# Optimization experiments

Hardware: AMD Instinct MI355X
Metric: run time of the kernel (lower is better)

The kernel has to match this reference:

```python
import jax, jax.numpy as jnp
import numpy as np

DIM = 1024
N_HEADS = 16
HEAD_DIM = DIM // N_HEADS
D_FF = 4096
EPS = 1e-6


def setup_inputs() -> dict:
    key = jax.random.key(0)
    ks = jax.random.split(key, 8)
    B, S = 2, 2048
    s = 0.02
    return {
        "x": jax.random.normal(ks[0], (B, S, DIM), dtype=jnp.float32),
        "mask": jnp.ones((B, 1, S, S), dtype=bool),
        "wq": jax.random.normal(ks[1], (DIM, DIM), dtype=jnp.float32) * s,
        "wk": jax.random.normal(ks[2], (DIM, DIM), dtype=jnp.float32) * s,
        "wv": jax.random.normal(ks[3], (DIM, DIM), dtype=jnp.float32) * s,
        "wo": jax.random.normal(ks[4], (DIM, DIM), dtype=jnp.float32) * s,
        "w_up": jax.random.normal(ks[5], (DIM, D_FF), dtype=jnp.float32) * s,
        "b_up": jnp.zeros((D_FF,), dtype=jnp.float32),
        "w_down": jax.random.normal(ks[6], (D_FF, DIM), dtype=jnp.float32) * s,
        "b_down": jnp.zeros((DIM,), dtype=jnp.float32),
        "ln1_a": jnp.ones((DIM,), dtype=jnp.float32),
        "ln1_b": jnp.zeros((DIM,), dtype=jnp.float32),
        "ln2_a": jnp.ones((DIM,), dtype=jnp.float32),
        "ln2_b": jnp.zeros((DIM,), dtype=jnp.float32),
    }


def _layernorm(x, alpha, bias):
    mu = jnp.mean(x, axis=-1, keepdims=True)
    # torch .std() is unbiased (ddof=1); denominator is (std + eps)
    sig = jnp.std(x, axis=-1, keepdims=True, ddof=1)
    return alpha * (x - mu) / (sig + EPS) + bias


def _attention(h, wq, wk, wv, wo):
    B, S, _ = h.shape
    q = (h @ wq).reshape(B, S, N_HEADS, HEAD_DIM).transpose(0, 2, 1, 3)
    k = (h @ wk).reshape(B, S, N_HEADS, HEAD_DIM).transpose(0, 2, 1, 3)
    v = (h @ wv).reshape(B, S, N_HEADS, HEAD_DIM).transpose(0, 2, 1, 3)
    scores = jnp.einsum("bhqd,bhkd->bhqk", q, k) / jnp.sqrt(jnp.float32(HEAD_DIM))
    # NOTE: original's masked_fill result is discarded -> mask is a no-op
    probs = jax.nn.softmax(scores, axis=-1)
    out = jnp.einsum("bhqk,bhkd->bhqd", probs, v)
    out = out.transpose(0, 2, 1, 3).reshape(B, S, DIM)
    return out @ wo


def reference(x, mask, wq, wk, wv, wo, w_up, b_up, w_down, b_down,
              ln1_a, ln1_b, ln2_a, ln2_b):
    h = _layernorm(x, ln1_a, ln1_b)
    x = x + _attention(h, wq, wk, wv, wo)
    h = _layernorm(x, ln2_a, ln2_b)
    ff = (jax.nn.relu(h @ w_up + b_up)) @ w_down + b_down
    return x + ff
```

## Files before the change

### kernel.cpp

```cpp
#include <hip/hip_runtime.h>
#include <hip/hip_bf16.h>

typedef __bf16 bf16_t;
typedef __bf16 bf16x8 __attribute__((ext_vector_type(8)));
typedef __bf16 bf16x4 __attribute__((ext_vector_type(4)));
typedef float  f32x4  __attribute__((ext_vector_type(4)));

#define DIM   1024
#define NHEAD 16
#define HD    64
#define DFF   4096
#define SEQ   2048
#define NTOK  4096

__device__ __forceinline__ void gl_lds16(const bf16_t* g, bf16_t* l) {
  __builtin_amdgcn_global_load_lds(
      (const __attribute__((address_space(1))) void*)g,
      (__attribute__((address_space(3))) void*)l, 16, 0, 0);
}

struct P4 { const float* a; const float* b; const float* c; const float* d; };

__global__ __launch_bounds__(256)
void transpose_cvt4(P4 in, bf16_t* __restrict__ out) {
  __shared__ bf16_t tile[32][33];
  const int z = blockIdx.z;
  const float* src = (z == 0) ? in.a : (z == 1) ? in.b : (z == 2) ? in.c : in.d;
  bf16_t* dst = out + (long)z * DIM * DIM;
  const int bx = blockIdx.x * 32, by = blockIdx.y * 32;
  const int t = threadIdx.x;
  const int r = t >> 3, c4 = (t & 7) * 4;
  f32x4 v = *(const f32x4*)&src[(long)(by + r) * DIM + bx + c4];
  tile[r][c4 + 0] = (bf16_t)v[0]; tile[r][c4 + 1] = (bf16_t)v[1];
  tile[r][c4 + 2] = (bf16_t)v[2]; tile[r][c4 + 3] = (bf16_t)v[3];
  __syncthreads();
  bf16x4 w;
  w[0] = tile[c4 + 0][r]; w[1] = tile[c4 + 1][r];
  w[2] = tile[c4 + 2][r]; w[3] = tile[c4 + 3][r];
  *(bf16x4*)&dst[(long)(bx + r) * DIM + by + c4] = w;
}

__global__ __launch_bounds__(256)
void transpose_cvt(const float* __restrict__ in, bf16_t* __restrict__ out,
                   int M, int N) {
  __shared__ bf16_t tile[32][33];
  const int bx = blockIdx.x * 32, by = blockIdx.y * 32;
  const int t = threadIdx.x;
  const int r = t >> 3, c4 = (t & 7) * 4;
  f32x4 v = *(const f32x4*)&in[(long)(by + r) * N + bx + c4];
  tile[r][c4 + 0] = (bf16_t)v[0]; tile[r][c4 + 1] = (bf16_t)v[1];
  tile[r][c4 + 2] = (bf16_t)v[2]; tile[r][c4 + 3] = (bf16_t)v[3];
  __syncthreads();
  bf16x4 w;
  w[0] = tile[c4 + 0][r]; w[1] = tile[c4 + 1][r];
  w[2] = tile[c4 + 2][r]; w[3] = tile[c4 + 3][r];
  *(bf16x4*)&out[(long)(bx + r) * M + by + c4] = w;
}

__global__ __launch_bounds__(256)
void layernorm_k(const float* __restrict__ x, const float* __restrict__ a,
                 const float* __restrict__ b, bf16_t* __restrict__ out) {
  const int row = blockIdx.x;
  const int t   = threadIdx.x;
  const float* xr = x + (long)row * DIM;
  f32x4 v = *(const f32x4*)&xr[t * 4];
  float s1 = v[0] + v[1] + v[2] + v[3];
  float s2 = v[0]*v[0] + v[1]*v[1] + v[2]*v[2] + v[3]*v[3];
  #pragma unroll
  for (int off = 32; off > 0; off >>= 1) {
    s1 += __shfl_down(s1, off);
    s2 += __shfl_down(s2, off);
  }
  __shared__ float r1[4], r2[4];
  if ((t & 63) == 0) { r1[t >> 6] = s1; r2[t >> 6] = s2; }
  __syncthreads();
  s1 = r1[0] + r1[1] + r1[2] + r1[3];
  s2 = r2[0] + r2[1] + r2[2] + r2[3];
  const float mu = s1 * (1.0f / DIM);
  float var = (s2 - (float)DIM * mu * mu) * (1.0f / (DIM - 1));
  var = fmaxf(var, 0.0f);
  const float inv = 1.0f / (sqrtf(var) + 1e-6f);
  f32x4 av = *(const f32x4*)&a[t * 4];
  f32x4 bv = *(const f32x4*)&b[t * 4];
  bf16x4 o;
  o[0] = (bf16_t)(av[0] * (v[0] - mu) * inv + bv[0]);
  o[1] = (bf16_t)(av[1] * (v[1] - mu) * inv + bv[1]);
  o[2] = (bf16_t)(av[2] * (v[2] - mu) * inv + bv[2]);
  o[3] = (bf16_t)(av[3] * (v[3] - mu) * inv + bv[3]);
  *(bf16x4*)&out[(long)row * DIM + t * 4] = o;
}

__global__ __launch_bounds__(256)
void layernorm_b(const bf16_t* __restrict__ x, const float* __restrict__ a,
                 const float* __restrict__ b, bf16_t* __restrict__ out) {
  const int row = blockIdx.x;
  const int t   = threadIdx.x;
  bf16x4 xv = *(const bf16x4*)&x[(long)row * DIM + t * 4];
  float v0 = (float)xv[0], v1 = (float)xv[1], v2 = (float)xv[2], v3 = (float)xv[3];
  float s1 = v0 + v1 + v2 + v3;
  float s2 = v0*v0 + v1*v1 + v2*v2 + v3*v3;
  #pragma unroll
  for (int off = 32; off > 0; off >>= 1) {
    s1 += __shfl_down(s1, off);
    s2 += __shfl_down(s2, off);
  }
  __shared__ float r1[4], r2[4];
  if ((t & 63) == 0) { r1[t >> 6] = s1; r2[t >> 6] = s2; }
  __syncthreads();
  s1 = r1[0] + r1[1] + r1[2] + r1[3];
  s2 = r2[0] + r2[1] + r2[2] + r2[3];
  const float mu = s1 * (1.0f / DIM);
  float var = (s2 - (float)DIM * mu * mu) * (1.0f / (DIM - 1));
  var = fmaxf(var, 0.0f);
  const float inv = 1.0f / (sqrtf(var) + 1e-6f);
  f32x4 av = *(const f32x4*)&a[t * 4];
  f32x4 bv = *(const f32x4*)&b[t * 4];
  bf16x4 o;
  o[0] = (bf16_t)(av[0] * (v0 - mu) * inv + bv[0]);
  o[1] = (bf16_t)(av[1] * (v1 - mu) * inv + bv[1]);
  o[2] = (bf16_t)(av[2] * (v2 - mu) * inv + bv[2]);
  o[3] = (bf16_t)(av[3] * (v3 - mu) * inv + bv[3]);
  *(bf16x4*)&out[(long)row * DIM + t * 4] = o;
}

__global__ __launch_bounds__(256)
void combine_att(const bf16_t* __restrict__ O1, const float* __restrict__ l0,
                 const float* __restrict__ l1, bf16_t* __restrict__ O0_attn) {
  const long i = ((long)blockIdx.x * 256 + threadIdx.x) * 4;
  const int n = (int)(i & (DIM - 1));
  const long t = i >> 10;
  const int h = n >> 6;
  const long lidx = ((t >> 11) * NHEAD + h) * SEQ + (t & (SEQ - 1));
  const float inv = 1.0f / (l0[lidx] + l1[lidx]);
  bf16x4 a = *(const bf16x4*)&O0_attn[i];
  bf16x4 b = *(const bf16x4*)&O1[i];
  bf16x4 o;
  o[0] = (bf16_t)(((float)a[0] + (float)b[0]) * inv);
  o[1] = (bf16_t)(((float)a[1] + (float)b[1]) * inv);
  o[2] = (bf16_t)(((float)a[2] + (float)b[2]) * inv);
  o[3] = (bf16_t)(((float)a[3] + (float)b[3]) * inv);
  *(bf16x4*)&O0_attn[i] = o;
}

__global__ __launch_bounds__(256)
void reduce_wo(const float* __restrict__ x, const bf16_t* __restrict__ p0,
               const bf16_t* __restrict__ p1, bf16_t* __restrict__ out) {
  const long i = ((long)blockIdx.x * 256 + threadIdx.x) * 4;
  f32x4 v = *(const f32x4*)&x[i];
  bf16x4 a = *(const bf16x4*)&p0[i];
  bf16x4 b = *(const bf16x4*)&p1[i];
  bf16x4 o;
  o[0] = (bf16_t)(v[0] + (float)a[0] + (float)b[0]);
  o[1] = (bf16_t)(v[1] + (float)a[1] + (float)b[1]);
  o[2] = (bf16_t)(v[2] + (float)a[2] + (float)b[2]);
  o[3] = (bf16_t)(v[3] + (float)a[3] + (float)b[3]);
  *(bf16x4*)&out[i] = o;
}

__global__ __launch_bounds__(256)
void reduce_fd(const bf16_t* __restrict__ x1b, const float* __restrict__ bias,
               const bf16_t* __restrict__ p0, const bf16_t* __restrict__ p1,
               float* __restrict__ out) {
  const long i = ((long)blockIdx.x * 256 + threadIdx.x) * 4;
  const int n = (int)(i & (DIM - 1));
  bf16x4 xv = *(const bf16x4*)&x1b[i];
  f32x4 bv = *(const f32x4*)&bias[n];
  bf16x4 a = *(const bf16x4*)&p0[i];
  bf16x4 b = *(const bf16x4*)&p1[i];
  f32x4 o;
  o[0] = (float)xv[0] + bv[0] + (float)a[0] + (float)b[0];
  o[1] = (float)xv[1] + bv[1] + (float)a[1] + (float)b[1];
  o[2] = (float)xv[2] + bv[2] + (float)a[2] + (float)b[2];
  o[3] = (float)xv[3] + bv[3] + (float)a[3] + (float)b[3];
  *(f32x4*)&out[i] = o;
}

enum { EPI_QKV = 1, EPI_BIAS_RELU = 3, EPI_PART = 6 };

#define BM 128
#define BK 32

template <int EPI, int TBN>
__global__ __launch_bounds__(256)
void gemm_bt(const bf16_t* __restrict__ A, int lda,
             const bf16_t* __restrict__ BT, int ldb,
             bf16_t* __restrict__ Cb, bf16_t* __restrict__ Cb2,
             const float* __restrict__ bias,
             int M, int N, int Ks) {
  __shared__ bf16_t sA[2][BM][BK];
  __shared__ bf16_t sB[2][TBN][BK];
  const int tid  = threadIdx.x;
  const int m0   = blockIdx.y * BM;
  const int n0   = blockIdx.x * TBN;
  const long koff = (long)blockIdx.z * Ks;
  const int lane = tid & 63, wave = tid >> 6;
  constexpr int MI = (TBN == 128) ? 4 : 2;
  const int wm = (TBN == 128) ? (wave >> 1) * 64 : wave * 32;
  const int wn = (TBN == 128) ? (wave & 1) * 64 : 0;
  const int fm = lane & 15, fq = lane >> 4;

  const int lr = lane >> 2, lc = (lane & 3) * 8;
  const bf16_t* gA0 = &A[(long)(m0 + wave * 32 + lr) * lda + koff + lc];
  const bf16_t* gA1 = gA0 + 16 * (long)lda;
  const int brow = (TBN == 128) ? wave * 32 : wave * 16;
  const bf16_t* gB0 = &BT[(long)(n0 + brow + lr) * ldb + koff + lc];
  const bf16_t* gB1 = gB0 + 16 * (long)ldb;

  f32x4 acc[MI][4] = {};

  gl_lds16(gA0, &sA[0][wave * 32][0]);
  gl_lds16(gA1, &sA[0][wave * 32 + 16][0]);
  gl_lds16(gB0, &sB[0][brow][0]);
  if (TBN == 128) gl_lds16(gB1, &sB[0][wave * 32 + 16][0]);
  gA0 += BK; gA1 += BK; gB0 += BK; gB1 += BK;

  int p = 0;
  for (int k0 = 0; k0 < Ks; k0 += BK, p ^= 1) {
    __syncthreads();
    if (k0 + BK < Ks) {
      gl_lds16(gA0, &sA[p ^ 1][wave * 32][0]);
      gl_lds16(gA1, &sA[p ^ 1][wave * 32 + 16][0]);
      gl_lds16(gB0, &sB[p ^ 1][brow][0]);
      if (TBN == 128) gl_lds16(gB1, &sB[p ^ 1][wave * 32 + 16][0]);
      gA0 += BK; gA1 += BK; gB0 += BK; gB1 += BK;
    }
    bf16x8 af[MI], bfr[4];
    #pragma unroll
    for (int i = 0; i < MI; i++) af[i]  = *(const bf16x8*)&sA[p][wm + i * 16 + fm][fq * 8];
    #pragma unroll
    for (int j = 0; j < 4; j++)  bfr[j] = *(const bf16x8*)&sB[p][wn + j * 16 + fm][fq * 8];
    #pragma unroll
    for (int i = 0; i < MI; i++)
      #pragma unroll
      for (int j = 0; j < 4; j++)
        acc[i][j] = __builtin_amdgcn_mfma_f32_16x16x32_bf16(af[i], bfr[j], acc[i][j], 0, 0, 0);
  }

  #pragma unroll
  for (int i = 0; i < MI; i++) {
    #pragma unroll
    for (int j = 0; j < 4; j++) {
      const int mb = m0 + wm + i * 16 + fq * 4;
      const int n  = n0 + wn + j * 16 + fm;
      #pragma unroll
      for (int r = 0; r < 4; r++) {
        const int m = mb + r;
        float vv = acc[i][j][r];
        if constexpr (EPI == EPI_QKV) {
          const int mat = n >> 10, h_ = (n >> 6) & 15, d_ = n & 63;
          const int b_ = m >> 11, s_ = m & 2047;
          if (mat == 2) {
            Cb2[((long)(b_ * NHEAD + h_) * HD + d_) * SEQ + s_] = (bf16_t)vv;
          } else {
            Cb[(long)mat * (32L * SEQ * HD) + (((long)(b_ * NHEAD + h_)) * SEQ + s_) * HD + d_] = (bf16_t)vv;
          }
        } else if constexpr (EPI == EPI_BIAS_RELU) {
          Cb[(long)m * N + n] = (bf16_t)fmaxf(vv + bias[n], 0.0f);
        } else {
          bf16_t* P = blockIdx.z ? Cb2 : Cb;
          P[(long)m * N + n] = (bf16_t)vv;
        }
      }
    }
  }
}

#define KVT 128

__device__ __forceinline__ int swz(int grp, int slot) {
  return (grp * 64 + (slot ^ ((slot >> 3) & 7) ^ (grp & 1))) * 8;
}

__global__ __launch_bounds__(256)
void flash_attn(const bf16_t* __restrict__ q, const bf16_t* __restrict__ k,
                const bf16_t* __restrict__ vt,
                bf16_t* __restrict__ O0, bf16_t* __restrict__ O1,
                float* __restrict__ l0, float* __restrict__ l1) {
  __shared__ bf16_t sK[16 * 64 * 8];
  __shared__ bf16_t sV[16 * 64 * 8];

  const int tid  = threadIdx.x;
  const int qb   = blockIdx.x & 15, bh = blockIdx.x >> 4;
  const int b    = bh >> 4, h = bh & 15;
  const int lane = tid & 63, wave = tid >> 6;
  const int fm   = lane & 15, fq = lane >> 4;
  const int qw0  = qb * 128 + wave * 32;
  const int kvbase = blockIdx.y * (SEQ / 2);
  bf16_t* Op = blockIdx.y ? O1 : O0;
  float*  lp = blockIdx.y ? l1 : l0;

  const bf16_t* qh  = q  + (long)bh * SEQ * HD;
  const bf16_t* kh  = k  + (long)bh * SEQ * HD;
  const bf16_t* vth = vt + (long)bh * HD * SEQ;

  bf16x8 bQ[2][2];
  #pragma unroll
  for (int qt = 0; qt < 2; qt++)
    #pragma unroll
    for (int kk = 0; kk < 2; kk++) {
      bf16x8 v = *(const bf16x8*)&qh[(long)(qw0 + qt * 16 + fm) * HD + kk * 32 + fq * 8];
      #pragma unroll
      for (int e = 0; e < 8; e++) v[e] = (bf16_t)((float)v[e] * 0.125f);
      bQ[qt][kk] = v;
    }

  float la = 0.f, lb = 0.f;
  f32x4 oA[4] = {}, oB[4] = {};

  for (int it = 0; it < (SEQ / 2) / KVT; it++) {
    const int kv0 = kvbase + it * KVT;
    __syncthreads();
    #pragma unroll
    for (int p = 0; p < 4; p++) {
      const int id = tid + p * 256;
      {
        const int rho = id >> 3, c0 = (id & 7) * 8;
        const int u = rho >> 5, w = rho & 31;
        const int h2 = (w >> 2) & 1;
        const int fmw = ((w >> 3) << 2) | (w & 3);
        const int kk = (id >> 2) & 1, fq3 = id & 3;
        bf16x8 g = *(const bf16x8*)&kh[(long)(kv0 + rho) * HD + c0];
        *(bf16x8*)&sK[swz((u * 2 + h2) * 2 + kk, fq3 * 16 + fmw)] = g;
      }
      {
        const int d = id >> 4, c0 = (id & 15) * 8;
        const int u = c0 >> 5, fq3 = (c0 >> 3) & 3;
        const int jd = d >> 4, fmw = d & 15;
        bf16x8 g = *(const bf16x8*)&vth[(long)d * SEQ + kv0 + c0];
        *(bf16x8*)&sV[swz(u * 4 + jd, fq3 * 16 + fmw)] = g;
      }
    }
    __syncthreads();

    #pragma unroll
    for (int u = 0; u < 4; u++) {
      f32x4 stA[2], stB[2];
      #pragma unroll
      for (int h2 = 0; h2 < 2; h2++) {
        bf16x8 aK0 = *(const bf16x8*)&sK[swz((u * 2 + h2) * 2 + 0, lane)];
        bf16x8 aK1 = *(const bf16x8*)&sK[swz((u * 2 + h2) * 2 + 1, lane)];
        f32x4 z0 = {};
        z0 = __builtin_amdgcn_mfma_f32_16x16x32_bf16(aK0, bQ[0][0], z0, 0, 0, 0);
        stA[h2] = __builtin_amdgcn_mfma_f32_16x16x32_bf16(aK1, bQ[0][1], z0, 0, 0, 0);
        f32x4 z1 = {};
        z1 = __builtin_amdgcn_mfma_f32_16x16x32_bf16(aK0, bQ[1][0], z1, 0, 0, 0);
        stB[h2] = __builtin_amdgcn_mfma_f32_16x16x32_bf16(aK1, bQ[1][1], z1, 0, 0, 0);
      }
      bf16x8 pA, pB;
      #pragma unroll
      for (int h2 = 0; h2 < 2; h2++)
        #pragma unroll
        for (int r = 0; r < 4; r++) {
          const float ea = __expf(stA[h2][r]);
          const float eb = __expf(stB[h2][r]);
          la += ea; lb += eb;
          pA[h2 * 4 + r] = (bf16_t)ea;
          pB[h2 * 4 + r] = (bf16_t)eb;
        }
      #pragma unroll
      for (int jd = 0; jd < 4; jd++) {
        bf16x8 bV = *(const bf16x8*)&sV[swz(u * 4 + jd, lane)];
        oA[jd] = __builtin_amdgcn_mfma_f32_16x16x32_bf16(pA, bV, oA[jd], 0, 0, 0);
        oB[jd] = __builtin_amdgcn_mfma_f32_16x16x32_bf16(pB, bV, oB[jd], 0, 0, 0);
      }
    }
  }

  la += __shfl_xor(la, 16); la += __shfl_xor(la, 32);
  lb += __shfl_xor(lb, 16); lb += __shfl_xor(lb, 32);
  if (fq == 0) {
    lp[(long)bh * SEQ + qw0 + fm]      = la;
    lp[(long)bh * SEQ + qw0 + 16 + fm] = lb;
  }

  #pragma unroll
  for (int r = 0; r < 4; r++) {
    const long rowA = ((long)b * SEQ + qw0 + fq * 4 + r) * DIM + h * HD;
    const long rowB = rowA + 16L * DIM;
    #pragma unroll
    for (int jd = 0; jd < 4; jd++) {
      Op[rowA + jd * 16 + fm] = (bf16_t)oA[jd][r];
      Op[rowB + jd * 16 + fm] = (bf16_t)oB[jd][r];
    }
  }
}

extern "C" void kernel_launch(void* const* d_in, const int* in_sizes, int n_in,
                              void* d_out, int out_size, void* d_ws, size_t ws_size,
                              hipStream_t stream) {
  (void)in_sizes; (void)n_in; (void)out_size; (void)ws_size;
  const float* x      = (const float*)d_in[0];
  const float* wq     = (const float*)d_in[2];
  const float* wk     = (const float*)d_in[3];
  const float* wv     = (const float*)d_in[4];
  const float* wo     = (const float*)d_in[5];
  const float* w_up   = (const float*)d_in[6];
  const float* b_up   = (const float*)d_in[7];
  const float* w_down = (const float*)d_in[8];
  const float* b_down = (const float*)d_in[9];
  const float* ln1a   = (const float*)d_in[10];
  const float* ln1b   = (const float*)d_in[11];
  const float* ln2a   = (const float*)d_in[12];
  const float* ln2b   = (const float*)d_in[13];

  char* ws = (char*)d_ws;
  const size_t MB = 1ull << 20;
  const size_t KB = 1ull << 10;
  float*  l0     = (float*)(ws);
  float*  l1     = (float*)(ws + 256 * KB);
  bf16_t* wqkvT  = (bf16_t*)(ws + 512 * KB);
  bf16_t* woT    = (bf16_t*)(ws + 512 * KB + 6 * MB);
  bf16_t* h      = (bf16_t*)(ws + 9 * MB);
  bf16_t* O0     = (bf16_t*)(ws + 9 * MB);
  bf16_t* attn   = (bf16_t*)(ws + 9 * MB);
  bf16_t* qkv    = (bf16_t*)(ws + 17 * MB);
  bf16_t* qd     = (bf16_t*)(ws + 17 * MB);
  bf16_t* kd     = (bf16_t*)(ws + 25 * MB);
  bf16_t* vtd    = (bf16_t*)(ws + 33 * MB);
  bf16_t* O1     = (bf16_t*)(ws + 41 * MB);
  bf16_t* p0_wo  = (bf16_t*)(ws + 17 * MB);
  bf16_t* p1_wo  = (bf16_t*)(ws + 25 * MB);
  bf16_t* x1b    = (bf16_t*)(ws + 41 * MB);
  bf16_t* h2     = (bf16_t*)(ws);
  bf16_t* wdownT = (bf16_t*)(ws + 49 * MB);
  bf16_t* wupT   = (bf16_t*)(ws + 57 * MB);
  bf16_t* ff1    = (bf16_t*)(ws + 9 * MB);
  bf16_t* p0_fd  = (bf16_t*)(ws);
  bf16_t* p1_fd  = (bf16_t*)(ws + 57 * MB);
  float*  outp   = (float*)d_out;

  const dim3 T(256);
  transpose_cvt4<<<dim3(32, 32, 4), T, 0, stream>>>(P4{wq, wk, wv, wo}, wqkvT);
  transpose_cvt<<<dim3(128, 32), T, 0, stream>>>(w_up, wupT, 1024, 4096);
  transpose_cvt<<<dim3(32, 128), T, 0, stream>>>(w_down, wdownT, 4096, 1024);

  layernorm_k<<<dim3(4096), T, 0, stream>>>(x, ln1a, ln1b, h);
  gemm_bt<EPI_QKV, 128><<<dim3(24, 32), T, 0, stream>>>(h, DIM, wqkvT, DIM, qkv, vtd,
                                                        nullptr, NTOK, 3072, DIM);
  flash_attn<<<dim3(512, 2), T, 0, stream>>>(qd, kd, vtd, O0, O1, l0, l1);
  combine_att<<<dim3(NTOK * DIM / 1024), T, 0, stream>>>(O1, l0, l1, attn);
  gemm_bt<EPI_PART, 64><<<dim3(16, 32, 2), T, 0, stream>>>(attn, DIM, woT, DIM, p0_wo, p1_wo,
                                                           nullptr, NTOK, DIM, DIM / 2);
  reduce_wo<<<dim3(NTOK * DIM / 1024), T, 0, stream>>>(x, p0_wo, p1_wo, x1b);
  layernorm_b<<<dim3(4096), T, 0, stream>>>(x1b, ln2a, ln2b, h2);
  gemm_bt<EPI_BIAS_RELU, 128><<<dim3(32, 32), T, 0, stream>>>(h2, DIM, wupT, DIM, ff1, nullptr,
                                                              b_up, NTOK, DFF, DIM);
  gemm_bt<EPI_PART, 64><<<dim3(16, 32, 2), T, 0, stream>>>(ff1, DFF, wdownT, DFF, p0_fd, p1_fd,
                                                           nullptr, NTOK, DIM, DFF / 2);
  reduce_fd<<<dim3(NTOK * DIM / 1024), T, 0, stream>>>(x1b, b_down, p0_fd, p1_fd, outp);
}
```

Before: 396.1 us.

## Register-staged GEMM prefetch and fuse Wo reduction with second layernorm

The GEMM main loop replaces direct global-to-LDS loads with loads into registers that are written to the alternate LDS buffer one iteration later, giving a two-stage prefetch and a single lgkm-wait-plus-barrier at the end of each iteration. Separately, the Wo partial-sum reduction and the second layernorm are merged into one per-row kernel, which removes a launch and a re-read of x1b. The register staging costs extra VGPRs and explicit LDS store instructions, and the hand-written waitcnt immediate must correctly cover outstanding LDS operations.

```diff
diff --git a/kernel.cpp b/kernel.cpp
--- a/kernel.cpp
+++ b/kernel.cpp
@@ -13,10 +13,9 @@
 #define SEQ   2048
 #define NTOK  4096
 
-__device__ __forceinline__ void gl_lds16(const bf16_t* g, bf16_t* l) {
-  __builtin_amdgcn_global_load_lds(
-      (const __attribute__((address_space(1))) void*)g,
-      (__attribute__((address_space(3))) void*)l, 16, 0, 0);
+__device__ __forceinline__ void lgkm_barrier() {
+  __builtin_amdgcn_s_waitcnt(0xC07F);
+  __builtin_amdgcn_s_barrier();
 }
 
 struct P4 { const float* a; const float* b; const float* c; const float* d; };
@@ -91,14 +90,25 @@
 }
 
 __global__ __launch_bounds__(256)
-void layernorm_b(const bf16_t* __restrict__ x, const float* __restrict__ a,
-                 const float* __restrict__ b, bf16_t* __restrict__ out) {
+void reduce_wo_ln(const float* __restrict__ x, const bf16_t* __restrict__ p0,
+                  const bf16_t* __restrict__ p1, const float* __restrict__ a,
+                  const float* __restrict__ b, bf16_t* __restrict__ x1b,
+                  bf16_t* __restrict__ h2) {
   const int row = blockIdx.x;
   const int t   = threadIdx.x;
-  bf16x4 xv = *(const bf16x4*)&x[(long)row * DIM + t * 4];
-  float v0 = (float)xv[0], v1 = (float)xv[1], v2 = (float)xv[2], v3 = (float)xv[3];
-  float s1 = v0 + v1 + v2 + v3;
-  float s2 = v0*v0 + v1*v1 + v2*v2 + v3*v3;
+  const long base = (long)row * DIM + t * 4;
+  f32x4 v = *(const f32x4*)&x[base];
+  bf16x4 pa = *(const bf16x4*)&p0[base];
+  bf16x4 pb = *(const bf16x4*)&p1[base];
+  bf16x4 xo;
+  xo[0] = (bf16_t)(v[0] + (float)pa[0] + (float)pb[0]);
+  xo[1] = (bf16_t)(v[1] + (float)pa[1] + (float)pb[1]);
+  xo[2] = (bf16_t)(v[2] + (float)pa[2] + (float)pb[2]);
+  xo[3] = (bf16_t)(v[3] + (float)pa[3] + (float)pb[3]);
+  *(bf16x4*)&x1b[base] = xo;
+  const float w0 = (float)xo[0], w1 = (float)xo[1], w2 = (float)xo[2], w3 = (float)xo[3];
+  float s1 = w0 + w1 + w2 + w3;
+  float s2 = w0*w0 + w1*w1 + w2*w2 + w3*w3;
   #pragma unroll
   for (int off = 32; off > 0; off >>= 1) {
     s1 += __shfl_down(s1, off);
@@ -116,11 +126,11 @@
   f32x4 av = *(const f32x4*)&a[t * 4];
   f32x4 bv = *(const f32x4*)&b[t * 4];
   bf16x4 o;
-  o[0] = (bf16_t)(av[0] * (v0 - mu) * inv + bv[0]);
-  o[1] = (bf16_t)(av[1] * (v1 - mu) * inv + bv[1]);
-  o[2] = (bf16_t)(av[2] * (v2 - mu) * inv + bv[2]);
-  o[3] = (bf16_t)(av[3] * (v3 - mu) * inv + bv[3]);
-  *(bf16x4*)&out[(long)row * DIM + t * 4] = o;
+  o[0] = (bf16_t)(av[0] * (w0 - mu) * inv + bv[0]);
+  o[1] = (bf16_t)(av[1] * (w1 - mu) * inv + bv[1]);
+  o[2] = (bf16_t)(av[2] * (w2 - mu) * inv + bv[2]);
+  o[3] = (bf16_t)(av[3] * (w3 - mu) * inv + bv[3]);
+  *(bf16x4*)&h2[(long)row * DIM + t * 4] = o;
 }
 
 __global__ __launch_bounds__(256)
@@ -143,21 +153,6 @@
 }
 
 __global__ __launch_bounds__(256)
-void reduce_wo(const float* __restrict__ x, const bf16_t* __restrict__ p0,
-               const bf16_t* __restrict__ p1, bf16_t* __restrict__ out) {
-  const long i = ((long)blockIdx.x * 256 + threadIdx.x) * 4;
-  f32x4 v = *(const f32x4*)&x[i];
-  bf16x4 a = *(const bf16x4*)&p0[i];
-  bf16x4 b = *(const bf16x4*)&p1[i];
-  bf16x4 o;
-  o[0] = (bf16_t)(v[0] + (float)a[0] + (float)b[0]);
-  o[1] = (bf16_t)(v[1] + (float)a[1] + (float)b[1]);
-  o[2] = (bf16_t)(v[2] + (float)a[2] + (float)b[2]);
-  o[3] = (bf16_t)(v[3] + (float)a[3] + (float)b[3]);
-  *(bf16x4*)&out[i] = o;
-}
-
-__global__ __launch_bounds__(256)
 void reduce_fd(const bf16_t* __restrict__ x1b, const float* __restrict__ bias,
                const bf16_t* __restrict__ p0, const bf16_t* __restrict__ p1,
                float* __restrict__ out) {
@@ -207,22 +202,40 @@
   const bf16_t* gB1 = gB0 + 16 * (long)ldb;
 
   f32x4 acc[MI][4] = {};
-
-  gl_lds16(gA0, &sA[0][wave * 32][0]);
-  gl_lds16(gA1, &sA[0][wave * 32 + 16][0]);
-  gl_lds16(gB0, &sB[0][brow][0]);
-  if (TBN == 128) gl_lds16(gB1, &sB[0][wave * 32 + 16][0]);
+  bf16x8 rA0, rA1, rB0, rB1;
+
+  rA0 = *(const bf16x8*)gA0;
+  rA1 = *(const bf16x8*)gA1;
+  rB0 = *(const bf16x8*)gB0;
+  if constexpr (TBN == 128) rB1 = *(const bf16x8*)gB1;
   gA0 += BK; gA1 += BK; gB0 += BK; gB1 += BK;
+  *(bf16x8*)&sA[0][wave * 32 + lr][lc]      = rA0;
+  *(bf16x8*)&sA[0][wave * 32 + 16 + lr][lc] = rA1;
+  *(bf16x8*)&sB[0][brow + lr][lc]           = rB0;
+  if constexpr (TBN == 128) *(bf16x8*)&sB[0][wave * 32 + 16 + lr][lc] = rB1;
+  if (BK < Ks) {
+    rA0 = *(const bf16x8*)gA0;
+    rA1 = *(const bf16x8*)gA1;
+    rB0 = *(const bf16x8*)gB0;
+    if constexpr (TBN == 128) rB1 = *(const bf16x8*)gB1;
+    gA0 += BK; gA1 += BK; gB0 += BK; gB1 += BK;
+  }
+  __syncthreads();
 
   int p = 0;
   for (int k0 = 0; k0 < Ks; k0 += BK, p ^= 1) {
-    __syncthreads();
     if (k0 + BK < Ks) {
-      gl_lds16(gA0, &sA[p ^ 1][wave * 32][0]);
-      gl_lds16(gA1, &sA[p ^ 1][wave * 32 + 16][0]);
-      gl_lds16(gB0, &sB[p ^ 1][brow][0]);
-      if (TBN == 128) gl_lds16(gB1, &sB[p ^ 1][wave * 32 + 16][0]);
-      gA0 += BK; gA1 += BK; gB0 += BK; gB1 += BK;
+      *(bf16x8*)&sA[p ^ 1][wave * 32 + lr][lc]      = rA0;
+      *(bf16x8*)&sA[p ^ 1][wave * 32 + 16 + lr][lc] = rA1;
+      *(bf16x8*)&sB[p ^ 1][brow + lr][lc]           = rB0;
+      if constexpr (TBN == 128) *(bf16x8*)&sB[p ^ 1][wave * 32 + 16 + lr][lc] = rB1;
+      if (k0 + 2 * BK < Ks) {
+        rA0 = *(const bf16x8*)gA0;
+        rA1 = *(const bf16x8*)gA1;
+        rB0 = *(const bf16x8*)gB0;
+        if constexpr (TBN == 128) rB1 = *(const bf16x8*)gB1;
+        gA0 += BK; gA1 += BK; gB0 += BK; gB1 += BK;
+      }
     }
     bf16x8 af[MI], bfr[4];
     #pragma unroll
@@ -234,6 +247,7 @@
       #pragma unroll
       for (int j = 0; j < 4; j++)
         acc[i][j] = __builtin_amdgcn_mfma_f32_16x16x32_bf16(af[i], bfr[j], acc[i][j], 0, 0, 0);
+    lgkm_barrier();
   }
 
   #pragma unroll
@@ -441,8 +455,7 @@
   combine_att<<<dim3(NTOK * DIM / 1024), T, 0, stream>>>(O1, l0, l1, attn);
   gemm_bt<EPI_PART, 64><<<dim3(16, 32, 2), T, 0, stream>>>(attn, DIM, woT, DIM, p0_wo, p1_wo,
                                                            nullptr, NTOK, DIM, DIM / 2);
-  reduce_wo<<<dim3(NTOK * DIM / 1024), T, 0, stream>>>(x, p0_wo, p1_wo, x1b);
-  layernorm_b<<<dim3(4096), T, 0, stream>>>(x1b, ln2a, ln2b, h2);
+  reduce_wo_ln<<<dim3(4096), T, 0, stream>>>(x, p0_wo, p1_wo, ln2a, ln2b, x1b, h2);
   gemm_bt<EPI_BIAS_RELU, 128><<<dim3(32, 32), T, 0, stream>>>(h2, DIM, wupT, DIM, ff1, nullptr,
                                                               b_up, NTOK, DFF, DIM);
   gemm_bt<EPI_PART, 64><<<dim3(16, 32, 2), T, 0, stream>>>(ff1, DFF, wdownT, DFF, p0_fd, p1_fd,
```

New measurement: 388.9 us. Within noise of the previous version (-1.8%).
